# Kernel tuning notes

Measured on AMD Instinct MI355X. Metric: run time of the kernel, lower is better.

## Reference

```python
import jax, jax.numpy as jnp
import numpy as np

B, T = 8, 32
C, H, W, P = 4, 84, 84, 14
GP = H // P              # 6 patches per side
LOBS = GP * GP           # 36 obs tokens per frame
S = LOBS + 3             # tokens per timestep (obs + R + a + r)
L = T * S                # 1248 total sequence length
D, NH, NL, DFF = 512, 8, 6, 2048
NRET, NACT, NREW = 120, 18, 3
NEG = -1e9


def _ln(x, g, b):
    m = x.mean(-1, keepdims=True)
    v = ((x - m) ** 2).mean(-1, keepdims=True)
    return (x - m) * jax.lax.rsqrt(v + 1e-5) * g + b


def _build_mask():
    # causal everywhere, but obs tokens within the same timestep attend bidirectionally
    pos = jnp.arange(L)
    step, off = pos // S, pos % S
    causal = pos[None, :] <= pos[:, None]
    is_obs = off < LOBS
    same_step = step[:, None] == step[None, :]
    obs_pair = is_obs[:, None] & is_obs[None, :] & same_step
    allowed = causal | obs_pair
    return jnp.where(allowed, 0.0, NEG).astype(jnp.float32)  # (L, L) additive


def _mha(x, Wqkv, bqkv, Wo, bo, mask):
    Bx, Lx, Dx = x.shape
    dh = Dx // NH
    qkv = x @ Wqkv + bqkv                       # (B, L, 3D)
    q, k, v = jnp.split(qkv, 3, axis=-1)
    sp = lambda t: t.reshape(Bx, Lx, NH, dh).transpose(0, 2, 1, 3)  # (B, H, L, dh)
    q, k, v = sp(q), sp(k), sp(v)
    scores = jnp.einsum('bhqd,bhkd->bhqk', q, k) / jnp.sqrt(jnp.float32(dh)) + mask
    attn = jax.nn.softmax(scores, axis=-1)
    o = jnp.einsum('bhqk,bhkd->bhqd', attn, v).transpose(0, 2, 1, 3).reshape(Bx, Lx, Dx)
    return o @ Wo + bo


def _forward(frames, rtg_bins, actions, reward_bins,
             patch_W, patch_b, return_E, action_E, reward_E, pos_E, type_E,
             Wqkv, bqkv, Wo, bo, ln1_g, ln1_b, ln2_g, ln2_b, W1, b1, W2, b2,
             hW_ret, hb_ret, hW_act, hb_act, hW_rew, hb_rew):
    # obs encoder: 14x14 patch embedding -> (B, T, LOBS, D)
    x = frames.reshape(B, T, C, GP, P, GP, P).transpose(0, 1, 3, 5, 2, 4, 6)
    x = x.reshape(B, T, LOBS, C * P * P)
    obs_tok = x @ patch_W + patch_b
    # interleave [obs..., R, a, r] per timestep
    step_tok = jnp.concatenate([
        obs_tok,
        return_E[rtg_bins][:, :, None, :],
        action_E[actions][:, :, None, :],
        reward_E[reward_bins][:, :, None, :],
    ], axis=2)                                   # (B, T, S, D)
    seq = step_tok.reshape(B, L, D)
    off = jnp.arange(L) % S
    type_ids = jnp.where(off < LOBS, 0, jnp.where(off == LOBS, 1, jnp.where(off == LOBS + 1, 2, 3)))
    seq = seq + pos_E + type_E[type_ids]
    mask = _build_mask()
    h = seq
    for i in range(NL):  # pre-norm transformer encoder, exact gelu
        h = h + _mha(_ln(h, ln1_g[i], ln1_b[i]), Wqkv[i], bqkv[i], Wo[i], bo[i], mask)
        hh = _ln(h, ln2_g[i], ln2_b[i])
        h = h + jax.nn.gelu(hh @ W1[i] + b1[i], approximate=False) @ W2[i] + b2[i]
    base = jnp.arange(T) * S
    ret_h = h[:, base + LOBS - 1]   # last obs token -> predicts R_t
    act_h = h[:, base + LOBS]       # R_t token -> predicts a_t
    rew_h = h[:, base + LOBS + 1]   # a_t token -> predicts r_t
    return (ret_h @ hW_ret + hb_ret, act_h @ hW_act + hb_act, rew_h @ hW_rew + hb_rew)


def setup_inputs() -> dict:
    key = jax.random.key(0)
    ks = jax.random.split(key, 24)
    s = 0.02
    inp = {}
    inp['frames'] = jax.random.normal(ks[0], (B, T, C, H, W), jnp.float32)
    inp['rtg_bins'] = jax.random.randint(ks[1], (B, T), 0, NRET)
    inp['actions'] = jax.random.randint(ks[2], (B, T), 0, NACT)
    inp['reward_bins'] = jax.random.randint(ks[3], (B, T), 0, NREW)
    inp['patch_W'] = jax.random.normal(ks[4], (C * P * P, D), jnp.float32) * s
    inp['patch_b'] = jnp.zeros((D,), jnp.float32)
    inp['return_E'] = jax.random.normal(ks[5], (NRET, D), jnp.float32) * s
    inp['action_E'] = jax.random.normal(ks[6], (NACT, D), jnp.float32) * s
    inp['reward_E'] = jax.random.normal(ks[7], (NREW, D), jnp.float32) * s
    inp['pos_E'] = jax.random.normal(ks[8], (L, D), jnp.float32) * s
    inp['type_E'] = jax.random.normal(ks[9], (4, D), jnp.float32) * s
    inp['Wqkv'] = jax.random.normal(ks[10], (NL, D, 3 * D), jnp.float32) * s
    inp['bqkv'] = jnp.zeros((NL, 3 * D), jnp.float32)
    inp['Wo'] = jax.random.normal(ks[11], (NL, D, D), jnp.float32) * s
    inp['bo'] = jnp.zeros((NL, D), jnp.float32)
    inp['ln1_g'] = jnp.ones((NL, D), jnp.float32)
    inp['ln1_b'] = jnp.zeros((NL, D), jnp.float32)
    inp['ln2_g'] = jnp.ones((NL, D), jnp.float32)
    inp['ln2_b'] = jnp.zeros((NL, D), jnp.float32)
    inp['W1'] = jax.random.normal(ks[12], (NL, D, DFF), jnp.float32) * s
    inp['b1'] = jnp.zeros((NL, DFF), jnp.float32)
    inp['W2'] = jax.random.normal(ks[13], (NL, DFF, D), jnp.float32) * s
    inp['b2'] = jnp.zeros((NL, D), jnp.float32)
    inp['hW_ret'] = jax.random.normal(ks[14], (D, NRET), jnp.float32) * s
    inp['hb_ret'] = jnp.zeros((NRET,), jnp.float32)
    inp['hW_act'] = jax.random.normal(ks[15], (D, NACT), jnp.float32) * s
    inp['hb_act'] = jnp.zeros((NACT,), jnp.float32)
    inp['hW_rew'] = jax.random.normal(ks[16], (D, NREW), jnp.float32) * s
    inp['hb_rew'] = jnp.zeros((NREW,), jnp.float32)
    return inp


def reference(frames, rtg_bins, actions, reward_bins,
              patch_W, patch_b, return_E, action_E, reward_E, pos_E, type_E,
              Wqkv, bqkv, Wo, bo, ln1_g, ln1_b, ln2_g, ln2_b, W1, b1, W2, b2,
              hW_ret, hb_ret, hW_act, hb_act, hW_rew, hb_rew):
    return _forward(frames, rtg_bins, actions, reward_bins,
                    patch_W, patch_b, return_E, action_E, reward_E, pos_E, type_E,
                    Wqkv, bqkv, Wo, bo, ln1_g, ln1_b, ln2_g, ln2_b, W1, b1, W2, b2,
                    hW_ret, hb_ret, hW_act, hb_act, hW_rew, hb_rew)
```

## Files before the change

kernel.cpp:

```cpp
#include <hip/hip_runtime.h>
#include <hip/hip_bf16.h>
#include <math.h>

typedef unsigned short ushort_t;
typedef __attribute__((ext_vector_type(8))) short bf16x8;
typedef __attribute__((ext_vector_type(4))) float floatx4;

#define B_   8
#define T_   32
#define C_   4
#define HW_  84
#define P_   14
#define GP_  6
#define LOBS 36
#define S_   39
#define L_   (T_ * S_)
#define D_   512
#define NH_  8
#define DH_  64
#define NL_  6
#define DFF_ 2048
#define NRET 120
#define NACT 18
#define NREW 3

#define ROWS (B_ * L_)
#define OBS_ROWS (B_ * T_ * LOBS)
#define PK   (C_ * P_ * P_)
#define PKP  800

#define OFF_H     0
#define OFF_AB1   5111808
#define OFF_AB2   (OFF_AB1 + 2555904)
#define OFF_QKVB  (OFF_AB2 + 2555904)
#define OFF_FFNB  (OFF_QKVB + 7667712)
#define OFF_WB    (OFF_FFNB + 10223616)
#define WS_FLOATS (OFF_WB + 9641984 + 16)

static __device__ __forceinline__ ushort_t f2b(float x) {
    union { float f; unsigned int u; } v; v.f = x;
    unsigned int r = v.u + 0x7FFFu + ((v.u >> 16) & 1u);
    return (ushort_t)(r >> 16);
}

static __device__ __forceinline__ void gload16(const ushort_t* g, ushort_t* l) {
    __builtin_amdgcn_global_load_lds(
        (const __attribute__((address_space(1))) void*)g,
        (__attribute__((address_space(3))) void*)l, 16, 0, 0);
}

__global__ void sentinel_kernel(float* out, int n) {
    int i = blockIdx.x * 256 + threadIdx.x;
    if (i < n) out[i] = 100.0f;
}

__global__ __launch_bounds__(256) void transpose_cvt_kernel(
    const float* __restrict__ src, ushort_t* __restrict__ dst, int K, int N)
{
    __shared__ float tile[32][33];
    int layer = blockIdx.z;
    int n0 = blockIdx.x * 32, k0 = blockIdx.y * 32;
    int tx = threadIdx.x & 31, ty = threadIdx.x >> 5;
    const float* s = src + (size_t)layer * K * N;
    ushort_t* d = dst + (size_t)layer * N * K;
#pragma unroll
    for (int r = 0; r < 32; r += 8)
        tile[ty + r][tx] = s[(size_t)(k0 + ty + r) * N + n0 + tx];
    __syncthreads();
#pragma unroll
    for (int r = 0; r < 32; r += 8)
        d[(size_t)(n0 + ty + r) * K + k0 + tx] = f2b(tile[tx][ty + r]);
}

__global__ __launch_bounds__(256) void transpose_patchw_kernel(
    const float* __restrict__ src, ushort_t* __restrict__ dst)
{
    __shared__ float tile[32][33];
    int n0 = blockIdx.x * 32, k0 = blockIdx.y * 32;
    int tx = threadIdx.x & 31, ty = threadIdx.x >> 5;
#pragma unroll
    for (int r = 0; r < 32; r += 8) {
        int k = k0 + ty + r;
        tile[ty + r][tx] = (k < PK) ? src[(size_t)k * D_ + n0 + tx] : 0.0f;
    }
    __syncthreads();
#pragma unroll
    for (int r = 0; r < 32; r += 8)
        dst[(size_t)(n0 + ty + r) * PKP + k0 + tx] = f2b(tile[tx][ty + r]);
}

__global__ void patchify_kernel(const float* __restrict__ frames, ushort_t* __restrict__ Xp) {
    int idx = blockIdx.x * 256 + threadIdx.x;
    if (idx >= OBS_ROWS * PKP) return;
    int r = idx / PKP, c = idx % PKP;
    if (c >= PK) { Xp[idx] = 0; return; }
    int bt = r / LOBS, p = r % LOBS;
    int gy = p / GP_, gx = p % GP_;
    int ch = c / (P_ * P_), rem = c % (P_ * P_);
    int py = rem / P_, px = rem % P_;
    size_t src = (((size_t)bt * C_ + ch) * HW_ + gy * P_ + py) * HW_ + gx * P_ + px;
    Xp[idx] = f2b(frames[src]);
}

__global__ __launch_bounds__(256) void gemm_mfma(
    const ushort_t* __restrict__ A, const ushort_t* __restrict__ BT,
    const float* __restrict__ bias, const float* __restrict__ residual,
    float* __restrict__ Cf, ushort_t* __restrict__ Cb,
    int M, int N, int K, int do_gelu)
{
    __shared__ ushort_t As[2][128 * 64];
    __shared__ ushort_t Bs[2][128 * 64];
    int t = threadIdx.x, lane = t & 63, w = t >> 6;

    int nx = gridDim.x;
    int nwg = nx * (int)gridDim.y;
    int orig = blockIdx.y * nx + blockIdx.x;
    int qq = nwg >> 3, rr = nwg & 7;
    int xcd = orig & 7, loc = orig >> 3;
    int wg = (xcd < rr ? xcd * (qq + 1) : rr * (qq + 1) + (xcd - rr) * qq) + loc;
    int row0 = (wg / nx) * 128, col0 = (wg % nx) * 128;

    int moff = (w & 1) << 6, noff = (w >> 1) << 6;
    int l16 = lane & 15, quad = lane >> 4;
    floatx4 acc[4][4];
#pragma unroll
    for (int i = 0; i < 4; ++i)
#pragma unroll
        for (int j = 0; j < 4; ++j) acc[i][j] = (floatx4){0.f, 0.f, 0.f, 0.f};

    int rsub = lane >> 3;
    int csw = (lane & 7) ^ rsub;
    const ushort_t* gA = A + (size_t)(row0 + w * 8 + rsub) * K + csw * 8;
    const ushort_t* gB = BT + (size_t)(col0 + w * 8 + rsub) * K + csw * 8;
    ushort_t* lA = &As[0][0] + w * 512;
    ushort_t* lB = &Bs[0][0] + w * 512;

    int nt = K >> 6;
#pragma unroll
    for (int s = 0; s < 4; ++s) {
        gload16(gA + (size_t)s * 32 * K, lA + s * 2048);
        gload16(gB + (size_t)s * 32 * K, lB + s * 2048);
    }

    int ch0 = (quad ^ (l16 & 7)) * 8;
    for (int kt = 0; kt < nt; ++kt) {
        int cur = kt & 1, nxt = cur ^ 1;
        if (kt + 1 < nt) {
            int k0n = (kt + 1) << 6;
#pragma unroll
            for (int s = 0; s < 4; ++s) {
                gload16(gA + (size_t)s * 32 * K + k0n, lA + nxt * 8192 + s * 2048);
                gload16(gB + (size_t)s * 32 * K + k0n, lB + nxt * 8192 + s * 2048);
            }
            asm volatile("s_waitcnt vmcnt(8)" ::: "memory");
        } else {
            asm volatile("s_waitcnt vmcnt(0)" ::: "memory");
        }
        __builtin_amdgcn_s_barrier();
        bf16x8 af0[4], af1[4], bf0[4], bf1[4];
#pragma unroll
        for (int i = 0; i < 4; ++i) {
            const ushort_t* pa = &As[cur][(moff + i * 16 + l16) * 64];
            af0[i] = *(const bf16x8*)(pa + ch0);
            af1[i] = *(const bf16x8*)(pa + (ch0 ^ 32));
        }
#pragma unroll
        for (int j = 0; j < 4; ++j) {
            const ushort_t* pb = &Bs[cur][(noff + j * 16 + l16) * 64];
            bf0[j] = *(const bf16x8*)(pb + ch0);
            bf1[j] = *(const bf16x8*)(pb + (ch0 ^ 32));
        }
        asm volatile("s_waitcnt lgkmcnt(0)" ::: "memory");
        __builtin_amdgcn_sched_barrier(0);
        __builtin_amdgcn_s_barrier();
#pragma unroll
        for (int i = 0; i < 4; ++i)
#pragma unroll
            for (int j = 0; j < 4; ++j) {
                acc[i][j] = __builtin_amdgcn_mfma_f32_16x16x32_bf16(af0[i], bf0[j], acc[i][j], 0, 0, 0);
                acc[i][j] = __builtin_amdgcn_mfma_f32_16x16x32_bf16(af1[i], bf1[j], acc[i][j], 0, 0, 0);
            }
    }
    if (K & 32) {
        int k0 = nt << 6;
        int n0i = (2 * w) * 64 + lane;
        int n1i = (2 * w + 1) * 64 + lane;
        gload16(A + (size_t)(row0 + (n0i >> 2)) * K + k0 + (n0i & 3) * 8, &As[0][0] + (2 * w) * 512);
        gload16(A + (size_t)(row0 + (n1i >> 2)) * K + k0 + (n1i & 3) * 8, &As[0][0] + (2 * w + 1) * 512);
        gload16(BT + (size_t)(col0 + (n0i >> 2)) * K + k0 + (n0i & 3) * 8, &Bs[0][0] + (2 * w) * 512);
        gload16(BT + (size_t)(col0 + (n1i >> 2)) * K + k0 + (n1i & 3) * 8, &Bs[0][0] + (2 * w + 1) * 512);
        asm volatile("s_waitcnt vmcnt(0)" ::: "memory");
        __builtin_amdgcn_s_barrier();
        bf16x8 af[4], bfv[4];
#pragma unroll
        for (int i = 0; i < 4; ++i)
            af[i] = *(const bf16x8*)&As[0][(moff + i * 16 + l16) * 32 + quad * 8];
#pragma unroll
        for (int j = 0; j < 4; ++j)
            bfv[j] = *(const bf16x8*)&Bs[0][(noff + j * 16 + l16) * 32 + quad * 8];
        asm volatile("s_waitcnt lgkmcnt(0)" ::: "memory");
        __builtin_amdgcn_sched_barrier(0);
#pragma unroll
        for (int i = 0; i < 4; ++i)
#pragma unroll
            for (int j = 0; j < 4; ++j)
                acc[i][j] = __builtin_amdgcn_mfma_f32_16x16x32_bf16(af[i], bfv[j], acc[i][j], 0, 0, 0);
    }
    int rquad = quad << 2;
#pragma unroll
    for (int j = 0; j < 4; ++j) {
        int col = col0 + noff + j * 16 + l16;
        float bv = bias ? bias[col] : 0.0f;
#pragma unroll
        for (int i = 0; i < 4; ++i) {
#pragma unroll
            for (int r = 0; r < 4; ++r) {
                int row = row0 + moff + i * 16 + rquad + r;
                float v = acc[i][j][r] + bv;
                if (do_gelu) v = 0.5f * v * (1.0f + erff(v * 0.70710678118654752f));
                if (residual) v += residual[(size_t)row * N + col];
                if (Cf) Cf[(size_t)row * N + col] = v;
                if (Cb) Cb[(size_t)row * N + col] = f2b(v);
            }
        }
    }
}

__global__ void assemble_kernel(const float* __restrict__ obs,
                                const int* __restrict__ rtg,
                                const int* __restrict__ act,
                                const int* __restrict__ rew,
                                const float* __restrict__ retE,
                                const float* __restrict__ actE,
                                const float* __restrict__ rewE,
                                const float* __restrict__ posE,
                                const float* __restrict__ typeE,
                                float* __restrict__ h) {
    int idx = blockIdx.x * 256 + threadIdx.x;
    if (idx >= ROWS * D_) return;
    int d = idx & (D_ - 1);
    int bl = idx / D_;
    int l = bl % L_, b = bl / L_;
    int t = l / S_, off = l % S_;
    int bt = b * T_ + t;
    float v;
    int ty;
    if (off < LOBS) {
        v = obs[((size_t)bt * LOBS + off) * D_ + d];
        ty = 0;
    } else if (off == LOBS) {
        v = retE[(size_t)rtg[bt] * D_ + d];
        ty = 1;
    } else if (off == LOBS + 1) {
        v = actE[(size_t)act[bt] * D_ + d];
        ty = 2;
    } else {
        v = rewE[(size_t)rew[bt] * D_ + d];
        ty = 3;
    }
    v += posE[(size_t)l * D_ + d] + typeE[(size_t)ty * D_ + d];
    h[idx] = v;
}

__global__ __launch_bounds__(256) void ln_fast(const float* __restrict__ x,
                                               const float* __restrict__ g,
                                               const float* __restrict__ bb,
                                               ushort_t* __restrict__ y) {
    int row = blockIdx.x;
    const float* xr = x + (size_t)row * D_;
    ushort_t* yr = y + (size_t)row * D_;
    int tid = threadIdx.x;
    float v0 = xr[tid], v1 = xr[tid + 256];
    __shared__ float red[4];
    int lane = tid & 63, wid = tid >> 6;
    float s = v0 + v1;
#pragma unroll
    for (int off = 32; off > 0; off >>= 1) s += __shfl_down(s, off, 64);
    if (lane == 0) red[wid] = s;
    __syncthreads();
    float mean = (red[0] + red[1] + red[2] + red[3]) * (1.0f / 512.0f);
    __syncthreads();
    float d0 = v0 - mean, d1 = v1 - mean;
    float vs = d0 * d0 + d1 * d1;
#pragma unroll
    for (int off = 32; off > 0; off >>= 1) vs += __shfl_down(vs, off, 64);
    if (lane == 0) red[wid] = vs;
    __syncthreads();
    float var = (red[0] + red[1] + red[2] + red[3]) * (1.0f / 512.0f);
    float rstd = rsqrtf(var + 1e-5f);
    yr[tid]       = f2b(d0 * rstd * g[tid]       + bb[tid]);
    yr[tid + 256] = f2b(d1 * rstd * g[tid + 256] + bb[tid + 256]);
}

__global__ __launch_bounds__(256) void vt_prep(const ushort_t* __restrict__ qkvb,
                                               ushort_t* __restrict__ vtg)
{
    __shared__ ushort_t tl[32][33];
    int bh = blockIdx.z; int b = bh >> 3, hh = bh & 7;
    int l0 = blockIdx.x * 32, d0 = blockIdx.y * 32;
    int tx = threadIdx.x & 31, ty = threadIdx.x >> 5;
#pragma unroll
    for (int r = 0; r < 32; r += 8)
        tl[ty + r][tx] = qkvb[((size_t)b * L_ + l0 + ty + r) * 1536 + 1024 + hh * 64 + d0 + tx];
    __syncthreads();
#pragma unroll
    for (int r = 0; r < 32; r += 8)
        vtg[((size_t)bh * 64 + d0 + ty + r) * L_ + l0 + tx] = tl[tx][ty + r];
}

__global__ __launch_bounds__(256) void attn_mfma(const ushort_t* __restrict__ qkvb,
                                                 const ushort_t* __restrict__ vtg,
                                                 ushort_t* __restrict__ outb)
{
    int bh = blockIdx.x; int hh = bh & 7, b = bh >> 3;
    int qt = 19 - blockIdx.y;
    int q0 = qt << 6;
    int t = threadIdx.x, lane = t & 63, w = t >> 6;
    int l16 = lane & 15, quad = lane >> 4;
    __shared__ ushort_t Ks[2][64 * 64];
    __shared__ ushort_t Vs[2][64 * 64];
    __shared__ ushort_t Ps[64][72];
    const ushort_t* base = qkvb + (size_t)b * (L_ * 1536);
    const ushort_t* vbase = vtg + (size_t)bh * 64 * L_;

    int qrow_l = q0 + w * 16 + l16; if (qrow_l >= L_) qrow_l = L_ - 1;
    const ushort_t* qp = base + (size_t)qrow_l * 1536 + hh * 64 + quad * 8;
    bf16x8 aq0 = *(const bf16x8*)qp;
    bf16x8 aq1 = *(const bf16x8*)(qp + 32);
    int qg[4], stepq[4], obsq[4];
#pragma unroll
    for (int r = 0; r < 4; ++r) {
        qg[r] = q0 + w * 16 + quad * 4 + r;
        stepq[r] = qg[r] / S_;
        obsq[r] = (qg[r] - stepq[r] * S_) < LOBS;
    }
    int qlast = q0 + 63; if (qlast > L_ - 1) qlast = L_ - 1;
    int kend_max = qlast;
    int we = (qlast / S_) * S_ + LOBS - 1;
    if (we > kend_max) kend_max = we;
    int ntiles = (kend_max >> 6) + 1;

    int sub = lane >> 3, jj = lane & 7;
    int jsw = jj ^ sub;
    int rk0 = (w << 4) + sub, rk1 = rk0 + 8;
    const ushort_t* kcol = base + 512 + hh * 64 + jsw * 8;
    const ushort_t* vr0 = vbase + (size_t)rk0 * L_;
    const ushort_t* vr1 = vbase + (size_t)rk1 * L_;
    ushort_t* ldsK0 = &Ks[0][0] + (w << 10);
    ushort_t* ldsK1 = ldsK0 + 512;
    ushort_t* ldsV0 = &Vs[0][0] + (w << 10);
    ushort_t* ldsV1 = ldsV0 + 512;

    gload16(kcol + (size_t)rk0 * 1536, ldsK0);
    gload16(kcol + (size_t)rk1 * 1536, ldsK1);
    gload16(vr0 + jsw * 8, ldsV0);
    gload16(vr1 + jsw * 8, ldsV1);
    __syncthreads();

    float psum[4] = {0.f, 0.f, 0.f, 0.f};
    floatx4 O[4];
#pragma unroll
    for (int nb = 0; nb < 4; ++nb) O[nb] = (floatx4){0.f, 0.f, 0.f, 0.f};

    int swz = (quad ^ (l16 & 7)) << 4;
    int buf = 0;
    for (int kt = 0; kt < ntiles; ++kt) {
        int nxt = buf ^ 1;
        if (kt + 1 < ntiles) {
            int k0n = (kt + 1) << 6;
            int g0 = k0n + rk0; if (g0 > L_ - 1) g0 = L_ - 1;
            int g1 = k0n + rk1; if (g1 > L_ - 1) g1 = L_ - 1;
            gload16(kcol + (size_t)g0 * 1536, ldsK0 + (nxt << 12));
            gload16(kcol + (size_t)g1 * 1536, ldsK1 + (nxt << 12));
            int cv = k0n + jsw * 8; if (cv > L_ - 8) cv = L_ - 8;
            gload16(vr0 + cv, ldsV0 + (nxt << 12));
            gload16(vr1 + cv, ldsV1 + (nxt << 12));
        }
        int k0 = kt << 6;
        const ushort_t* Kb = &Ks[0][0] + (buf << 12);
        const ushort_t* Vb = &Vs[0][0] + (buf << 12);
        floatx4 sc4[4];
#pragma unroll
        for (int nb = 0; nb < 4; ++nb) {
            const char* kp = (const char*)(Kb + ((nb * 16 + l16) << 6));
            bf16x8 bk0 = *(const bf16x8*)(kp + swz);
            bf16x8 bk1 = *(const bf16x8*)(kp + (swz ^ 64));
            floatx4 z = (floatx4){0.f, 0.f, 0.f, 0.f};
            z = __builtin_amdgcn_mfma_f32_16x16x32_bf16(aq0, bk0, z, 0, 0, 0);
            z = __builtin_amdgcn_mfma_f32_16x16x32_bf16(aq1, bk1, z, 0, 0, 0);
            sc4[nb] = z;
        }
        if (kt < qt) {
#pragma unroll
            for (int nb = 0; nb < 4; ++nb)
#pragma unroll
                for (int r = 0; r < 4; ++r) {
                    float p = __expf(sc4[nb][r] * 0.125f);
                    psum[r] += p;
                    Ps[w * 16 + quad * 4 + r][nb * 16 + l16] = f2b(p);
                }
        } else {
#pragma unroll
            for (int nb = 0; nb < 4; ++nb) {
                int kg = k0 + nb * 16 + l16;
                int stepk = kg / S_;
                int kobs = (kg - stepk * S_) < LOBS;
#pragma unroll
                for (int r = 0; r < 4; ++r) {
                    int allowed = (kg <= qg[r]) || (obsq[r] && kobs && (stepk == stepq[r]));
                    float p = allowed ? __expf(sc4[nb][r] * 0.125f) : 0.0f;
                    psum[r] += p;
                    Ps[w * 16 + quad * 4 + r][nb * 16 + l16] = f2b(p);
                }
            }
        }
        bf16x8 ap0 = *(const bf16x8*)&Ps[w * 16 + l16][quad * 8];
        bf16x8 ap1 = *(const bf16x8*)&Ps[w * 16 + l16][quad * 8 + 32];
#pragma unroll
        for (int nb = 0; nb < 4; ++nb) {
            const char* vp = (const char*)(Vb + ((nb * 16 + l16) << 6));
            bf16x8 bv0 = *(const bf16x8*)(vp + swz);
            bf16x8 bv1 = *(const bf16x8*)(vp + (swz ^ 64));
            O[nb] = __builtin_amdgcn_mfma_f32_16x16x32_bf16(ap0, bv0, O[nb], 0, 0, 0);
            O[nb] = __builtin_amdgcn_mfma_f32_16x16x32_bf16(ap1, bv1, O[nb], 0, 0, 0);
        }
        __syncthreads();
        buf = nxt;
    }
#pragma unroll
    for (int off = 1; off < 16; off <<= 1)
#pragma unroll
        for (int r = 0; r < 4; ++r)
            psum[r] += __shfl_xor(psum[r], off, 64);
#pragma unroll
    for (int r = 0; r < 4; ++r) {
        if (qg[r] < L_) {
            float inv = 1.0f / psum[r];
#pragma unroll
            for (int nb = 0; nb < 4; ++nb)
                outb[((size_t)b * L_ + qg[r]) * 512 + hh * 64 + nb * 16 + l16] =
                    f2b(O[nb][r] * inv);
        }
    }
}

__global__ __launch_bounds__(256) void heads_fast(const float* __restrict__ h,
                            const float* __restrict__ hW_ret, const float* __restrict__ hb_ret,
                            const float* __restrict__ hW_act, const float* __restrict__ hb_act,
                            const float* __restrict__ hW_rew, const float* __restrict__ hb_rew,
                            float* __restrict__ out) {
    int bt = blockIdx.x;
    int b = bt >> 5, t = bt & 31;
    __shared__ float hr[D_], ha[D_], hw[D_];
    size_t base = ((size_t)b * L_ + (size_t)t * S_) * D_;
    int tid = threadIdx.x;
    for (int i = tid; i < D_; i += 256) {
        hr[i] = h[base + (size_t)(LOBS - 1) * D_ + i];
        ha[i] = h[base + (size_t)LOBS * D_ + i];
        hw[i] = h[base + (size_t)(LOBS + 1) * D_ + i];
    }
    __syncthreads();
    if (tid < NRET) {
        float acc = hb_ret[tid];
#pragma unroll 16
        for (int k = 0; k < D_; ++k) acc = fmaf(hr[k], hW_ret[(size_t)k * NRET + tid], acc);
        out[(size_t)bt * NRET + tid] = acc;
    } else if (tid < NRET + NACT) {
        int n = tid - NRET;
        float acc = hb_act[n];
#pragma unroll 16
        for (int k = 0; k < D_; ++k) acc = fmaf(ha[k], hW_act[(size_t)k * NACT + n], acc);
        out[(size_t)(B_ * T_ * NRET) + (size_t)bt * NACT + n] = acc;
    } else if (tid < NRET + NACT + NREW) {
        int n = tid - NRET - NACT;
        float acc = hb_rew[n];
#pragma unroll 16
        for (int k = 0; k < D_; ++k) acc = fmaf(hw[k], hW_rew[(size_t)k * NREW + n], acc);
        out[(size_t)(B_ * T_ * (NRET + NACT)) + (size_t)bt * NREW + n] = acc;
    }
}

static inline int cdiv_i(long long a, int b) { return (int)((a + b - 1) / b); }

extern "C" void kernel_launch(void* const* d_in, const int* in_sizes, int n_in,
                              void* d_out, int out_size, void* d_ws, size_t ws_size,
                              hipStream_t stream) {
    if (ws_size < (size_t)WS_FLOATS * sizeof(float)) {
        sentinel_kernel<<<(out_size + 255) / 256, 256, 0, stream>>>((float*)d_out, out_size);
        return;
    }
    const float* frames  = (const float*)d_in[0];
    const int*   rtg     = (const int*)d_in[1];
    const int*   actions = (const int*)d_in[2];
    const int*   rewards = (const int*)d_in[3];

    float* ws   = (float*)d_ws;
    float* h    = ws + OFF_H;
    ushort_t* ab1  = (ushort_t*)(ws + OFF_AB1);
    ushort_t* ab2  = (ushort_t*)(ws + OFF_AB2);
    ushort_t* qkvb = (ushort_t*)(ws + OFF_QKVB);
    ushort_t* ffnb = (ushort_t*)(ws + OFF_FFNB);
    ushort_t* vtg  = (ushort_t*)(ws + OFF_FFNB);
    ushort_t* xpb  = (ushort_t*)(ws + OFF_FFNB);
    float*    obs  = ws + OFF_FFNB + 3686400;
    ushort_t* wpatchT = (ushort_t*)(ws + OFF_WB);
    ushort_t* wqkvT = wpatchT + PKP * D_;
    ushort_t* woT   = wqkvT + NL_ * D_ * 3 * D_;
    ushort_t* w1T   = woT + NL_ * D_ * D_;
    ushort_t* w2T   = w1T + NL_ * D_ * DFF_;

    transpose_patchw_kernel<<<dim3(16, 25), 256, 0, stream>>>((const float*)d_in[4], wpatchT);
    transpose_cvt_kernel<<<dim3(48, 16, NL_), 256, 0, stream>>>((const float*)d_in[11], wqkvT, D_, 3 * D_);
    transpose_cvt_kernel<<<dim3(16, 16, NL_), 256, 0, stream>>>((const float*)d_in[13], woT, D_, D_);
    transpose_cvt_kernel<<<dim3(64, 16, NL_), 256, 0, stream>>>((const float*)d_in[19], w1T, D_, DFF_);
    transpose_cvt_kernel<<<dim3(16, 64, NL_), 256, 0, stream>>>((const float*)d_in[21], w2T, DFF_, D_);

    patchify_kernel<<<cdiv_i((long long)OBS_ROWS * PKP, 256), 256, 0, stream>>>(frames, xpb);
    gemm_mfma<<<dim3(D_ / 128, OBS_ROWS / 128), 256, 0, stream>>>(
        xpb, wpatchT, (const float*)d_in[5], nullptr, obs, nullptr, OBS_ROWS, D_, PKP, 0);

    assemble_kernel<<<cdiv_i((long long)ROWS * D_, 256), 256, 0, stream>>>(
        obs, rtg, actions, rewards,
        (const float*)d_in[6], (const float*)d_in[7], (const float*)d_in[8],
        (const float*)d_in[9], (const float*)d_in[10], h);

    for (int i = 0; i < NL_; ++i) {
        ln_fast<<<ROWS, 256, 0, stream>>>(h, (const float*)d_in[15] + i * D_,
                                          (const float*)d_in[16] + i * D_, ab1);
        gemm_mfma<<<dim3(3 * D_ / 128, ROWS / 128), 256, 0, stream>>>(
            ab1, wqkvT + (size_t)i * D_ * 3 * D_, (const float*)d_in[12] + i * 3 * D_,
            nullptr, nullptr, qkvb, ROWS, 3 * D_, D_, 0);
        vt_prep<<<dim3(39, 2, 64), 256, 0, stream>>>(qkvb, vtg);
        attn_mfma<<<dim3(64, 20), 256, 0, stream>>>(qkvb, vtg, ab2);
        gemm_mfma<<<dim3(D_ / 128, ROWS / 128), 256, 0, stream>>>(
            ab2, woT + (size_t)i * D_ * D_, (const float*)d_in[14] + i * D_,
            h, h, nullptr, ROWS, D_, D_, 0);
        ln_fast<<<ROWS, 256, 0, stream>>>(h, (const float*)d_in[17] + i * D_,
                                          (const float*)d_in[18] + i * D_, ab1);
        gemm_mfma<<<dim3(DFF_ / 128, ROWS / 128), 256, 0, stream>>>(
            ab1, w1T + (size_t)i * D_ * DFF_, (const float*)d_in[20] + i * DFF_,
            nullptr, nullptr, ffnb, ROWS, DFF_, D_, 1);
        gemm_mfma<<<dim3(D_ / 128, ROWS / 128), 256, 0, stream>>>(
            ffnb, w2T + (size_t)i * DFF_ * D_, (const float*)d_in[22] + i * D_,
            h, h, nullptr, ROWS, D_, DFF_, 0);
    }

    heads_fast<<<B_ * T_, 256, 0, stream>>>(h,
        (const float*)d_in[23], (const float*)d_in[24],
        (const float*)d_in[25], (const float*)d_in[26],
        (const float*)d_in[27], (const float*)d_in[28], (float*)d_out);
}
```

Measured before the change: 1.635 ms.

## Halve GEMM N-tile, add MFMA priority hints, use polynomial GELU

Result: faster. 1.446 ms (-11.6%).

```diff
diff --git a/kernel.cpp b/kernel.cpp
--- a/kernel.cpp
+++ b/kernel.cpp
@@ -43,6 +43,18 @@
     return (ushort_t)(r >> 16);
 }
 
+static __device__ __forceinline__ float gelu_f(float v) {
+    float z = fabsf(v) * 0.70710678118654752f;
+    float t = 1.0f / (1.0f + 0.3275911f * z);
+    float p = fmaf(t, 1.061405429f, -1.453152027f);
+    p = fmaf(t, p, 1.421413741f);
+    p = fmaf(t, p, -0.284496736f);
+    p = fmaf(t, p, 0.254829592f);
+    float e = 1.0f - p * t * __expf(-z * z);
+    float s = v < 0.0f ? -e : e;
+    return 0.5f * v * (1.0f + s);
+}
+
 static __device__ __forceinline__ void gload16(const ushort_t* g, ushort_t* l) {
     __builtin_amdgcn_global_load_lds(
         (const __attribute__((address_space(1))) void*)g,
@@ -109,7 +121,7 @@
     int M, int N, int K, int do_gelu)
 {
     __shared__ ushort_t As[2][128 * 64];
-    __shared__ ushort_t Bs[2][128 * 64];
+    __shared__ ushort_t Bs[2][64 * 64];
     int t = threadIdx.x, lane = t & 63, w = t >> 6;
 
     int nx = gridDim.x;
@@ -118,15 +130,15 @@
     int qq = nwg >> 3, rr = nwg & 7;
     int xcd = orig & 7, loc = orig >> 3;
     int wg = (xcd < rr ? xcd * (qq + 1) : rr * (qq + 1) + (xcd - rr) * qq) + loc;
-    int row0 = (wg / nx) * 128, col0 = (wg % nx) * 128;
-
-    int moff = (w & 1) << 6, noff = (w >> 1) << 6;
+    int row0 = (wg / nx) * 128, col0 = (wg % nx) * 64;
+
+    int moff = (w & 1) << 6, noff = (w >> 1) << 5;
     int l16 = lane & 15, quad = lane >> 4;
-    floatx4 acc[4][4];
+    floatx4 acc[4][2];
 #pragma unroll
     for (int i = 0; i < 4; ++i)
 #pragma unroll
-        for (int j = 0; j < 4; ++j) acc[i][j] = (floatx4){0.f, 0.f, 0.f, 0.f};
+        for (int j = 0; j < 2; ++j) acc[i][j] = (floatx4){0.f, 0.f, 0.f, 0.f};
 
     int rsub = lane >> 3;
     int csw = (lane & 7) ^ rsub;
@@ -137,10 +149,9 @@
 
     int nt = K >> 6;
 #pragma unroll
-    for (int s = 0; s < 4; ++s) {
-        gload16(gA + (size_t)s * 32 * K, lA + s * 2048);
-        gload16(gB + (size_t)s * 32 * K, lB + s * 2048);
-    }
+    for (int s = 0; s < 4; ++s) gload16(gA + (size_t)s * 32 * K, lA + s * 2048);
+#pragma unroll
+    for (int s = 0; s < 2; ++s) gload16(gB + (size_t)s * 32 * K, lB + s * 2048);
 
     int ch0 = (quad ^ (l16 & 7)) * 8;
     for (int kt = 0; kt < nt; ++kt) {
@@ -148,16 +159,17 @@
         if (kt + 1 < nt) {
             int k0n = (kt + 1) << 6;
 #pragma unroll
-            for (int s = 0; s < 4; ++s) {
+            for (int s = 0; s < 4; ++s)
                 gload16(gA + (size_t)s * 32 * K + k0n, lA + nxt * 8192 + s * 2048);
-                gload16(gB + (size_t)s * 32 * K + k0n, lB + nxt * 8192 + s * 2048);
-            }
-            asm volatile("s_waitcnt vmcnt(8)" ::: "memory");
+#pragma unroll
+            for (int s = 0; s < 2; ++s)
+                gload16(gB + (size_t)s * 32 * K + k0n, lB + nxt * 4096 + s * 2048);
+            asm volatile("s_waitcnt vmcnt(6)" ::: "memory");
         } else {
             asm volatile("s_waitcnt vmcnt(0)" ::: "memory");
         }
         __builtin_amdgcn_s_barrier();
-        bf16x8 af0[4], af1[4], bf0[4], bf1[4];
+        bf16x8 af0[4], af1[4], bf0[2], bf1[2];
 #pragma unroll
         for (int i = 0; i < 4; ++i) {
             const ushort_t* pa = &As[cur][(moff + i * 16 + l16) * 64];
@@ -165,7 +177,7 @@
             af1[i] = *(const bf16x8*)(pa + (ch0 ^ 32));
         }
 #pragma unroll
-        for (int j = 0; j < 4; ++j) {
+        for (int j = 0; j < 2; ++j) {
             const ushort_t* pb = &Bs[cur][(noff + j * 16 + l16) * 64];
             bf0[j] = *(const bf16x8*)(pb + ch0);
             bf1[j] = *(const bf16x8*)(pb + (ch0 ^ 32));
@@ -173,42 +185,44 @@
         asm volatile("s_waitcnt lgkmcnt(0)" ::: "memory");
         __builtin_amdgcn_sched_barrier(0);
         __builtin_amdgcn_s_barrier();
+        __builtin_amdgcn_s_setprio(1);
 #pragma unroll
         for (int i = 0; i < 4; ++i)
 #pragma unroll
-            for (int j = 0; j < 4; ++j) {
+            for (int j = 0; j < 2; ++j) {
                 acc[i][j] = __builtin_amdgcn_mfma_f32_16x16x32_bf16(af0[i], bf0[j], acc[i][j], 0, 0, 0);
                 acc[i][j] = __builtin_amdgcn_mfma_f32_16x16x32_bf16(af1[i], bf1[j], acc[i][j], 0, 0, 0);
             }
+        __builtin_amdgcn_s_setprio(0);
     }
     if (K & 32) {
         int k0 = nt << 6;
-        int n0i = (2 * w) * 64 + lane;
-        int n1i = (2 * w + 1) * 64 + lane;
-        gload16(A + (size_t)(row0 + (n0i >> 2)) * K + k0 + (n0i & 3) * 8, &As[0][0] + (2 * w) * 512);
-        gload16(A + (size_t)(row0 + (n1i >> 2)) * K + k0 + (n1i & 3) * 8, &As[0][0] + (2 * w + 1) * 512);
-        gload16(BT + (size_t)(col0 + (n0i >> 2)) * K + k0 + (n0i & 3) * 8, &Bs[0][0] + (2 * w) * 512);
-        gload16(BT + (size_t)(col0 + (n1i >> 2)) * K + k0 + (n1i & 3) * 8, &Bs[0][0] + (2 * w + 1) * 512);
+        int g0 = 2 * w * 64 + lane;
+        int g1 = (2 * w + 1) * 64 + lane;
+        gload16(A + (size_t)(row0 + (g0 >> 2)) * K + k0 + (g0 & 3) * 8, &As[0][0] + 2 * w * 512);
+        gload16(A + (size_t)(row0 + (g1 >> 2)) * K + k0 + (g1 & 3) * 8, &As[0][0] + (2 * w + 1) * 512);
+        int gb = w * 64 + lane;
+        gload16(BT + (size_t)(col0 + (gb >> 2)) * K + k0 + (gb & 3) * 8, &Bs[0][0] + w * 512);
         asm volatile("s_waitcnt vmcnt(0)" ::: "memory");
         __builtin_amdgcn_s_barrier();
-        bf16x8 af[4], bfv[4];
+        bf16x8 af[4], bfv[2];
 #pragma unroll
         for (int i = 0; i < 4; ++i)
             af[i] = *(const bf16x8*)&As[0][(moff + i * 16 + l16) * 32 + quad * 8];
 #pragma unroll
-        for (int j = 0; j < 4; ++j)
+        for (int j = 0; j < 2; ++j)
             bfv[j] = *(const bf16x8*)&Bs[0][(noff + j * 16 + l16) * 32 + quad * 8];
         asm volatile("s_waitcnt lgkmcnt(0)" ::: "memory");
         __builtin_amdgcn_sched_barrier(0);
 #pragma unroll
         for (int i = 0; i < 4; ++i)
 #pragma unroll
-            for (int j = 0; j < 4; ++j)
+            for (int j = 0; j < 2; ++j)
                 acc[i][j] = __builtin_amdgcn_mfma_f32_16x16x32_bf16(af[i], bfv[j], acc[i][j], 0, 0, 0);
     }
     int rquad = quad << 2;
 #pragma unroll
-    for (int j = 0; j < 4; ++j) {
+    for (int j = 0; j < 2; ++j) {
         int col = col0 + noff + j * 16 + l16;
         float bv = bias ? bias[col] : 0.0f;
 #pragma unroll
@@ -217,7 +231,7 @@
             for (int r = 0; r < 4; ++r) {
                 int row = row0 + moff + i * 16 + rquad + r;
                 float v = acc[i][j][r] + bv;
-                if (do_gelu) v = 0.5f * v * (1.0f + erff(v * 0.70710678118654752f));
+                if (do_gelu) v = gelu_f(v);
                 if (residual) v += residual[(size_t)row * N + col];
                 if (Cf) Cf[(size_t)row * N + col] = v;
                 if (Cb) Cb[(size_t)row * N + col] = f2b(v);
@@ -380,6 +394,7 @@
         const ushort_t* Kb = &Ks[0][0] + (buf << 12);
         const ushort_t* Vb = &Vs[0][0] + (buf << 12);
         floatx4 sc4[4];
+        __builtin_amdgcn_s_setprio(1);
 #pragma unroll
         for (int nb = 0; nb < 4; ++nb) {
             const char* kp = (const char*)(Kb + ((nb * 16 + l16) << 6));
@@ -390,6 +405,7 @@
             z = __builtin_amdgcn_mfma_f32_16x16x32_bf16(aq1, bk1, z, 0, 0, 0);
             sc4[nb] = z;
         }
+        __builtin_amdgcn_s_setprio(0);
         if (kt < qt) {
 #pragma unroll
             for (int nb = 0; nb < 4; ++nb)
@@ -416,6 +432,7 @@
         }
         bf16x8 ap0 = *(const bf16x8*)&Ps[w * 16 + l16][quad * 8];
         bf16x8 ap1 = *(const bf16x8*)&Ps[w * 16 + l16][quad * 8 + 32];
+        __builtin_amdgcn_s_setprio(1);
 #pragma unroll
         for (int nb = 0; nb < 4; ++nb) {
             const char* vp = (const char*)(Vb + ((nb * 16 + l16) << 6));
@@ -424,6 +441,7 @@
             O[nb] = __builtin_amdgcn_mfma_f32_16x16x32_bf16(ap0, bv0, O[nb], 0, 0, 0);
             O[nb] = __builtin_amdgcn_mfma_f32_16x16x32_bf16(ap1, bv1, O[nb], 0, 0, 0);
         }
+        __builtin_amdgcn_s_setprio(0);
         __syncthreads();
         buf = nxt;
     }
@@ -516,7 +534,7 @@
     transpose_cvt_kernel<<<dim3(16, 64, NL_), 256, 0, stream>>>((const float*)d_in[21], w2T, DFF_, D_);
 
     patchify_kernel<<<cdiv_i((long long)OBS_ROWS * PKP, 256), 256, 0, stream>>>(frames, xpb);
-    gemm_mfma<<<dim3(D_ / 128, OBS_ROWS / 128), 256, 0, stream>>>(
+    gemm_mfma<<<dim3(D_ / 64, OBS_ROWS / 128), 256, 0, stream>>>(
         xpb, wpatchT, (const float*)d_in[5], nullptr, obs, nullptr, OBS_ROWS, D_, PKP, 0);
 
     assemble_kernel<<<cdiv_i((long long)ROWS * D_, 256), 256, 0, stream>>>(
@@ -527,20 +545,20 @@
     for (int i = 0; i < NL_; ++i) {
         ln_fast<<<ROWS, 256, 0, stream>>>(h, (const float*)d_in[15] + i * D_,
                                           (const float*)d_in[16] + i * D_, ab1);
-        gemm_mfma<<<dim3(3 * D_ / 128, ROWS / 128), 256, 0, stream>>>(
+        gemm_mfma<<<dim3(3 * D_ / 64, ROWS / 128), 256, 0, stream>>>(
             ab1, wqkvT + (size_t)i * D_ * 3 * D_, (const float*)d_in[12] + i * 3 * D_,
             nullptr, nullptr, qkvb, ROWS, 3 * D_, D_, 0);
         vt_prep<<<dim3(39, 2, 64), 256, 0, stream>>>(qkvb, vtg);
         attn_mfma<<<dim3(64, 20), 256, 0, stream>>>(qkvb, vtg, ab2);
-        gemm_mfma<<<dim3(D_ / 128, ROWS / 128), 256, 0, stream>>>(
+        gemm_mfma<<<dim3(D_ / 64, ROWS / 128), 256, 0, stream>>>(
             ab2, woT + (size_t)i * D_ * D_, (const float*)d_in[14] + i * D_,
             h, h, nullptr, ROWS, D_, D_, 0);
         ln_fast<<<ROWS, 256, 0, stream>>>(h, (const float*)d_in[17] + i * D_,
                                           (const float*)d_in[18] + i * D_, ab1);
-        gemm_mfma<<<dim3(DFF_ / 128, ROWS / 128), 256, 0, stream>>>(
+        gemm_mfma<<<dim3(DFF_ / 64, ROWS / 128), 256, 0, stream>>>(
             ab1, w1T + (size_t)i * D_ * DFF_, (const float*)d_in[20] + i * DFF_,
             nullptr, nullptr, ffnb, ROWS, DFF_, D_, 1);
-        gemm_mfma<<<dim3(D_ / 128, ROWS / 128), 256, 0, stream>>>(
+        gemm_mfma<<<dim3(D_ / 64, ROWS / 128), 256, 0, stream>>>(
             ffnb, w2T + (size_t)i * DFF_ * D_, (const float*)d_in[22] + i * D_,
             h, h, nullptr, ROWS, D_, DFF_, 0);
     }
```
